# Kernel optimization log

Hardware: AMD Instinct MI355X
Metric: run time of the kernel (lower is better)

The kernel has to match this reference:

```python
import jax, jax.numpy as jnp
import numpy as np

N, F_IN, HID, HEADS, E, G, CLS = 20000, 128, 32, 8, 320000, 64, 10


def setup_inputs() -> dict:
    key = jax.random.key(0)
    ks = jax.random.split(key, 16)
    HC = HEADS * HID
    inp = {
        'x': jax.random.normal(ks[0], (N, F_IN), jnp.float32),
        'edge_index': jax.random.randint(ks[1], (2, E), 0, N, jnp.int64),
        'batch': jnp.sort(jax.random.randint(ks[2], (N,), 0, G, jnp.int64)),
        'W1': jax.random.normal(ks[3], (F_IN, HC), jnp.float32) * 0.1,
        'att_l1': jax.random.normal(ks[4], (HEADS, HID), jnp.float32) * 0.1,
        'att_r1': jax.random.normal(ks[5], (HEADS, HID), jnp.float32) * 0.1,
        'b1': jnp.zeros((HC,), jnp.float32),
        'W2': jax.random.normal(ks[6], (HC, HC), jnp.float32) * 0.1,
        'att_l2': jax.random.normal(ks[7], (HEADS, HID), jnp.float32) * 0.1,
        'att_r2': jax.random.normal(ks[8], (HEADS, HID), jnp.float32) * 0.1,
        'b2': jnp.zeros((HC,), jnp.float32),
        'lin_W': jax.random.normal(ks[9], (HC, CLS), jnp.float32) * 0.1,
        'lin_b': jnp.zeros((CLS,), jnp.float32),
    }
    return inp


def _add_self_loops(edge_index):
    loops = jnp.arange(N, dtype=edge_index.dtype)
    return (jnp.concatenate([edge_index[0], loops]),
            jnp.concatenate([edge_index[1], loops]))


def _supergat_conv(x, edge_index, W, att_l, att_r, b):
    # SuperGATConv, attention_type='MX', eval mode (no dropout / neg sampling)
    h = (x @ W).reshape(-1, HEADS, HID)          # [N, H, C]
    src, dst = _add_self_loops(edge_index)       # j -> i
    x_j = h[src]                                 # [Etot, H, C]
    x_i = h[dst]
    logits = jnp.einsum('ehc,ehc->eh', x_i, x_j)            # dot-product part
    alpha = jnp.einsum('ehc,hc->eh', x_j, att_l) + jnp.einsum('ehc,hc->eh', x_i, att_r)
    alpha = alpha * jax.nn.sigmoid(logits)
    alpha = jax.nn.leaky_relu(alpha, 0.2)
    # segment softmax over incoming edges of each dst node
    amax = jax.ops.segment_max(alpha, dst, num_segments=N)
    ex = jnp.exp(alpha - amax[dst])
    denom = jax.ops.segment_sum(ex, dst, num_segments=N)
    attn = ex / (denom[dst] + 1e-16)             # [Etot, H]
    out = jax.ops.segment_sum(x_j * attn[..., None], dst, num_segments=N)  # [N,H,C]
    return out.reshape(-1, HEADS * HID) + b


def reference(x, edge_index, batch, W1, att_l1, att_r1, b1, W2, att_l2, att_r2, b2, lin_W, lin_b):
    h = _supergat_conv(x, edge_index, W1, att_l1, att_r1, b1)
    h = jax.nn.elu(h)
    h = _supergat_conv(h, edge_index, W2, att_l2, att_r2, b2)
    # global mean pool over graphs
    sums = jax.ops.segment_sum(h, batch, num_segments=G)
    cnts = jax.ops.segment_sum(jnp.ones((h.shape[0], 1), h.dtype), batch, num_segments=G)
    pooled = sums / jnp.maximum(cnts, 1.0)
    return pooled @ lin_W + lin_b
```

## Files before the change

kernel.cpp:

```cpp
#include <hip/hip_runtime.h>
#include <hip/hip_bf16.h>
#include <math.h>

#define NNODE 20000
#define FIN   128
#define HC    256
#define HEADS 8
#define HID   32
#define NEDGE 320000
#define NGRAPH 64
#define NCLS  10
#define MAXDEG 64

typedef __attribute__((ext_vector_type(8))) short short8v;
typedef __attribute__((ext_vector_type(8))) unsigned short ushort8v;
typedef __attribute__((ext_vector_type(4))) float float4v;

__device__ __forceinline__ ushort f2bf(float f) {
    __hip_bfloat16 b = __float2bfloat16(f);
    return *(ushort*)&b;
}
__device__ __forceinline__ float bf2f(ushort u) {
    return __uint_as_float(((unsigned)u) << 16);
}


#define ZB_DEG ((NNODE + 255) / 256)
#define ZB_BND ((NNODE + 255) / 256)
#define ZB_PS  ((NGRAPH * HC + 255) / 256)

__global__ __launch_bounds__(256) void init_kernel(const float* __restrict__ W1,
                                                   const float* __restrict__ W2,
                                                   const int* __restrict__ batch,
                                                   ushort* __restrict__ W1t,
                                                   ushort* __restrict__ W2t,
                                                   int* __restrict__ deg,
                                                   int* __restrict__ gstart,
                                                   float* __restrict__ psum) {
    int b = blockIdx.x;
    if (b < 128) {
        int e = b * 256 + threadIdx.x;
        int k = e >> 8, n = e & 255;
        W1t[(long)n * FIN + k] = f2bf(W1[(long)k * 256 + n]);
    } else if (b < 384) {
        int e = (b - 128) * 256 + threadIdx.x;
        int k = e >> 8, n = e & 255;
        W2t[(long)n * HC + k] = f2bf(W2[(long)k * 256 + n]);
    } else if (b < 384 + ZB_DEG) {
        int i = (b - 384) * 256 + threadIdx.x;
        if (i < NNODE) deg[i] = 0;
    } else if (b < 384 + ZB_DEG + ZB_BND) {
        int i = (b - 384 - ZB_DEG) * 256 + threadIdx.x;
        if (i < NNODE) {
            int bi = batch[i];
            if (i == 0) {
                for (int g = 0; g <= bi; g++) gstart[g] = 0;
            } else {
                int bp = batch[i - 1];
                for (int g = bp + 1; g <= bi; g++) gstart[g] = i;
            }
            if (i == NNODE - 1) {
                for (int g = bi + 1; g <= NGRAPH; g++) gstart[g] = NNODE;
            }
        }
    } else {
        int i = (b - 384 - ZB_DEG - ZB_BND) * 256 + threadIdx.x;
        if (i < NGRAPH * HC) psum[i] = 0.f;
    }
}


__global__ __launch_bounds__(256) void fill_slots(const int* __restrict__ ei,
                                                  int* __restrict__ deg,
                                                  ushort* __restrict__ esrc) {
    int e = blockIdx.x * blockDim.x + threadIdx.x;
    if (e >= NEDGE) return;
    int src = ei[e];
    int dst = ei[NEDGE + e];
    int slot = atomicAdd(&deg[dst], 1);
    if (slot < MAXDEG) esrc[dst * MAXDEG + slot] = (ushort)src;
}


template<bool A_FP32>
__global__ __launch_bounds__(256) void gemm_mfma(const void* __restrict__ Aptr,
                                                 const ushort* __restrict__ Bt,
                                                 ushort* __restrict__ C,
                                                 const float* __restrict__ attL,
                                                 const float* __restrict__ attR,
                                                 float* __restrict__ aL,
                                                 float* __restrict__ aR,
                                                 int M, int K) {
    __shared__ __align__(16) ushort As[64][72];
    __shared__ __align__(16) ushort Bs[64][72];
    int tid = threadIdx.x;
    int rowBase = blockIdx.x * 64;
    int colBase = blockIdx.y * 64;
    int wave = tid >> 6;
    int l = tid & 63;
    int lm = l & 15;
    int quad = l >> 4;
    int r0 = (wave >> 1) * 32;
    int c0 = (wave & 1) * 32;

    float4v acc00 = {0.f, 0.f, 0.f, 0.f};
    float4v acc01 = acc00, acc10 = acc00, acc11 = acc00;

    float4  af[4];
    short8v ab[2];
    short8v bb[2];

    auto load_tile = [&](int k0) {
        if constexpr (A_FP32) {
            const float* A = (const float*)Aptr;
            #pragma unroll
            for (int q = 0; q < 4; q++) {
                int idx = tid + q * 256;
                int r   = idx >> 4;
                int kc  = (idx & 15) * 4;
                int grow = rowBase + r;
                float4 v = make_float4(0.f, 0.f, 0.f, 0.f);
                if (grow < M) v = *(const float4*)(A + (long)grow * K + k0 + kc);
                af[q] = v;
            }
        } else {
            const ushort* A = (const ushort*)Aptr;
            #pragma unroll
            for (int q = 0; q < 2; q++) {
                int ch = tid + q * 256;
                int r  = ch >> 3;
                int kc = (ch & 7) * 8;
                int grow = rowBase + r;
                short8v av = {};
                if (grow < M) av = *(const short8v*)(A + (long)grow * K + k0 + kc);
                ab[q] = av;
            }
        }
        #pragma unroll
        for (int q = 0; q < 2; q++) {
            int ch = tid + q * 256;
            int r  = ch >> 3;
            int kc = (ch & 7) * 8;
            bb[q] = *(const short8v*)(Bt + (long)(colBase + r) * K + k0 + kc);
        }
    };

    auto store_tile = [&]() {
        if constexpr (A_FP32) {
            #pragma unroll
            for (int q = 0; q < 4; q++) {
                int idx = tid + q * 256;
                int r   = idx >> 4;
                int kc  = (idx & 15) * 4;
                float4 v = af[q];
                ushort4 o = { f2bf(v.x), f2bf(v.y), f2bf(v.z), f2bf(v.w) };
                *(ushort4*)&As[r][kc] = o;
            }
        } else {
            #pragma unroll
            for (int q = 0; q < 2; q++) {
                int ch = tid + q * 256;
                int r  = ch >> 3;
                int kc = (ch & 7) * 8;
                *(short8v*)&As[r][kc] = ab[q];
            }
        }
        #pragma unroll
        for (int q = 0; q < 2; q++) {
            int ch = tid + q * 256;
            int r  = ch >> 3;
            int kc = (ch & 7) * 8;
            *(short8v*)&Bs[r][kc] = bb[q];
        }
    };

    load_tile(0);
    for (int k0 = 0; k0 < K; k0 += 64) {
        store_tile();
        __syncthreads();
        if (k0 + 64 < K) load_tile(k0 + 64);
        #pragma unroll
        for (int ks = 0; ks < 64; ks += 32) {
            int kb = ks + quad * 8;
            short8v a0 = *(const short8v*)&As[r0 + lm][kb];
            short8v a1 = *(const short8v*)&As[r0 + 16 + lm][kb];
            short8v b0 = *(const short8v*)&Bs[c0 + lm][kb];
            short8v b1 = *(const short8v*)&Bs[c0 + 16 + lm][kb];
            acc00 = __builtin_amdgcn_mfma_f32_16x16x32_bf16(a0, b0, acc00, 0, 0, 0);
            acc01 = __builtin_amdgcn_mfma_f32_16x16x32_bf16(a0, b1, acc01, 0, 0, 0);
            acc10 = __builtin_amdgcn_mfma_f32_16x16x32_bf16(a1, b0, acc10, 0, 0, 0);
            acc11 = __builtin_amdgcn_mfma_f32_16x16x32_bf16(a1, b1, acc11, 0, 0, 0);
        }
        __syncthreads();
    }

    int cb = colBase + c0;
    int hd = cb >> 5;
    float al0 = attL[cb + lm], al1 = attL[cb + 16 + lm];
    float ar0 = attR[cb + lm], ar1 = attR[cb + 16 + lm];
    #pragma unroll
    for (int mi = 0; mi < 2; mi++) {
        float4v s0 = mi ? acc10 : acc00;
        float4v s1 = mi ? acc11 : acc01;
        #pragma unroll
        for (int r = 0; r < 4; r++) {
            int row = rowBase + r0 + mi * 16 + quad * 4 + r;
            float pl = s0[r] * al0 + s1[r] * al1;
            float pr = s0[r] * ar0 + s1[r] * ar1;
            #pragma unroll
            for (int s2 = 1; s2 < 16; s2 <<= 1) {
                pl += __shfl_xor(pl, s2);
                pr += __shfl_xor(pr, s2);
            }
            if (row < M) {
                C[(long)row * 256 + cb + lm]      = f2bf(s0[r]);
                C[(long)row * 256 + cb + 16 + lm] = f2bf(s1[r]);
                if (lm == 0) {
                    aL[row * 8 + hd] = pl;
                    aR[row * 8 + hd] = pr;
                }
            }
        }
    }
}


template<int FUSE_POOL>
__global__ __launch_bounds__(256, 8) void fused_attn(const ushort* __restrict__ h,
                                                     const int* __restrict__ degv,
                                                     const ushort* __restrict__ esrc,
                                                     const float* __restrict__ aL,
                                                     const float* __restrict__ aR,
                                                     const float* __restrict__ bias,
                                                     ushort* __restrict__ out,
                                                     float* __restrict__ psum,
                                                     const int* __restrict__ batch,
                                                     int apply_elu) {
    __shared__ float sh[4][HC];
    __shared__ int sgid[4];
    int wave = threadIdx.x >> 6;
    int node = blockIdx.x * 4 + wave;
    int l = threadIdx.x & 63;
    int slot = l >> 5;
    int lh = l & 31;
    int head = lh >> 2;

    if (FUSE_POOL && l == 0) sgid[wave] = batch[node];

    const ushort8v* h8 = (const ushort8v*)h;
    ushort8v hiu = h8[(long)node * 32 + lh];
    float a_ri = aR[node * 8 + head];
    float a_li = aL[node * 8 + head];
    int beg = node * MAXDEG;
    int deg = min(degv[node], MAXDEG);

    int p  = slot;
    int j0 = (p     < deg) ? (int)esrc[beg + p]     : 0;
    int j1 = (p + 2 < deg) ? (int)esrc[beg + p + 2] : 0;
    int j2 = (p + 4 < deg) ? (int)esrc[beg + p + 4] : 0;
    ushort8v hb0 = h8[(long)j0 * 32 + lh];
    float    ab0 = aL[j0 * 8 + head];
    ushort8v hb1 = h8[(long)j1 * 32 + lh];
    float    ab1 = aL[j1 * 8 + head];

    float prod_s = 0.f;
    #pragma unroll
    for (int c = 0; c < 8; c++) {
        float v = bf2f(hiu[c]);
        prod_s = fmaf(v, v, prod_s);
    }
    prod_s += __shfl_xor(prod_s, 1);
    prod_s += __shfl_xor(prod_s, 2);
    float alpha_s = (a_li + a_ri) * __builtin_amdgcn_rcpf(1.f + __expf(-prod_s));
    alpha_s = (alpha_s > 0.f) ? alpha_s : 0.2f * alpha_s;
    float ex_s = (slot == 0) ? __expf(alpha_s) : 0.f;

    float lsum = ex_s;
    float acc[8];
    #pragma unroll
    for (int c = 0; c < 8; c++) acc[c] = ex_s * bf2f(hiu[c]);

    for (; p < deg; p += 2) {
        ushort8v hb2 = h8[(long)j2 * 32 + lh];
        float    ab2 = aL[j2 * 8 + head];
        int j3 = (p + 6 < deg) ? (int)esrc[beg + p + 6] : 0;

        float hj[8];
        float prod = 0.f;
        #pragma unroll
        for (int c = 0; c < 8; c++) {
            hj[c] = bf2f(hb0[c]);
            prod = fmaf(bf2f(hiu[c]), hj[c], prod);
        }
        prod += __shfl_xor(prod, 1);
        prod += __shfl_xor(prod, 2);
        float alpha = (ab0 + a_ri) * __builtin_amdgcn_rcpf(1.f + __expf(-prod));
        alpha = (alpha > 0.f) ? alpha : 0.2f * alpha;
        float ex = __expf(alpha);
        lsum += ex;
        #pragma unroll
        for (int c = 0; c < 8; c++) acc[c] += ex * hj[c];

        hb0 = hb1; ab0 = ab1;
        hb1 = hb2; ab1 = ab2;
        j2  = j3;
    }

    lsum += __shfl_xor(lsum, 32);
    #pragma unroll
    for (int c = 0; c < 8; c++) acc[c] += __shfl_xor(acc[c], 32);

    if (slot == 0) {
        float inv = __builtin_amdgcn_rcpf(lsum + 1e-16f);
        float4 b0 = ((const float4*)bias)[lh * 2];
        float4 b1 = ((const float4*)bias)[lh * 2 + 1];
        float bb[8] = {b0.x, b0.y, b0.z, b0.w, b1.x, b1.y, b1.z, b1.w};
        if (FUSE_POOL) {
            #pragma unroll
            for (int c = 0; c < 8; c++)
                sh[wave][lh * 8 + c] = acc[c] * inv + bb[c];
        } else {
            ushort8v o;
            #pragma unroll
            for (int c = 0; c < 8; c++) {
                float r = acc[c] * inv + bb[c];
                if (apply_elu) r = (r > 0.f) ? r : (__expf(r) - 1.f);
                o[c] = f2bf(r);
            }
            *(ushort8v*)(out + (long)node * 256 + lh * 8) = o;
        }
    }

    if (FUSE_POOL) {
        __syncthreads();
        int t = threadIdx.x;
        float v = sh[0][t];
        int g0 = sgid[0];
        #pragma unroll
        for (int w2 = 1; w2 < 4; w2++) {
            int gw = sgid[w2];
            if (gw == g0) v += sh[w2][t];
            else { atomicAdd(&psum[g0 * HC + t], v); g0 = gw; v = sh[w2][t]; }
        }
        atomicAdd(&psum[g0 * HC + t], v);
    }
}


__global__ __launch_bounds__(256) void final2(const float* __restrict__ psum,
                                              const int* __restrict__ gstart,
                                              const float* __restrict__ linW,
                                              const float* __restrict__ linb,
                                              float* __restrict__ out) {
    int g = blockIdx.x;
    int t = threadIdx.x;
    __shared__ float pooled[HC];
    float cnt = fmaxf((float)(gstart[g + 1] - gstart[g]), 1.f);
    pooled[t] = psum[g * HC + t] / cnt;
    __syncthreads();
    if (t < NCLS) {
        float o = linb[t];
        for (int c = 0; c < HC; c++) o += pooled[c] * linW[c * NCLS + t];
        out[g * NCLS + t] = o;
    }
}


extern "C" void kernel_launch(void* const* d_in, const int* in_sizes, int n_in,
                              void* d_out, int out_size, void* d_ws, size_t ws_size,
                              hipStream_t stream) {
    const float* x     = (const float*)d_in[0];
    const int*   ei    = (const int*)d_in[1];
    const int*   batch = (const int*)d_in[2];
    const float* W1    = (const float*)d_in[3];
    const float* attL1 = (const float*)d_in[4];
    const float* attR1 = (const float*)d_in[5];
    const float* b1    = (const float*)d_in[6];
    const float* W2    = (const float*)d_in[7];
    const float* attL2 = (const float*)d_in[8];
    const float* attR2 = (const float*)d_in[9];
    const float* b2    = (const float*)d_in[10];
    const float* linW  = (const float*)d_in[11];
    const float* linb  = (const float*)d_in[12];
    float* out = (float*)d_out;

    char* w = (char*)d_ws;
    size_t o = 0;
    int* deg      = (int*)(w + o); o += (size_t)NNODE * 4;
    o = (o + 15) & ~(size_t)15;
    ushort* esrc  = (ushort*)(w + o); o += (size_t)NNODE * MAXDEG * 2;
    o = (o + 15) & ~(size_t)15;
    ushort* W1t = (ushort*)(w + o); o += (size_t)FIN * HC * 2;
    ushort* W2t = (ushort*)(w + o); o += (size_t)HC * HC * 2;
    o = (o + 15) & ~(size_t)15;
    ushort* hbA = (ushort*)(w + o); o += (size_t)NNODE * HC * 2;
    ushort* hbB = (ushort*)(w + o); o += (size_t)NNODE * HC * 2;
    o = (o + 15) & ~(size_t)15;
    float* aL   = (float*)(w + o); o += (size_t)NNODE * HEADS * 4;
    float* aR   = (float*)(w + o); o += (size_t)NNODE * HEADS * 4;
    o = (o + 15) & ~(size_t)15;
    float* psum = (float*)(w + o); o += (size_t)NGRAPH * HC * 4;
    int* gstart = (int*)(w + o); o += 80 * 4;

    init_kernel<<<384 + ZB_DEG + ZB_BND + ZB_PS, 256, 0, stream>>>(
        W1, W2, batch, W1t, W2t, deg, gstart, psum);

    int eb = (NEDGE + 255) / 256;
    fill_slots<<<eb, 256, 0, stream>>>(ei, deg, esrc);

    dim3 gg((NNODE + 63) / 64, HC / 64);
    int ab = (NNODE + 3) / 4;
    gemm_mfma<true><<<gg, 256, 0, stream>>>(x, W1t, hbA, attL1, attR1, aL, aR, NNODE, FIN);
    fused_attn<0><<<ab, 256, 0, stream>>>(hbA, deg, esrc, aL, aR, b1, hbB, nullptr, batch, 1);
    gemm_mfma<false><<<gg, 256, 0, stream>>>(hbB, W2t, hbA, attL2, attR2, aL, aR, NNODE, HC);
    fused_attn<1><<<ab, 256, 0, stream>>>(hbA, deg, esrc, aL, aR, b2, nullptr, psum, batch, 0);
    final2<<<NGRAPH, 256, 0, stream>>>(psum, gstart, linW, linb, out);
}
```

Baseline: 195.1 us.

## Widen GEMM tile to full 256 columns and deepen attention gather prefetch

```diff
diff --git a/kernel.cpp b/kernel.cpp
--- a/kernel.cpp
+++ b/kernel.cpp
@@ -92,23 +92,26 @@
                                                  float* __restrict__ aR,
                                                  int M, int K) {
     __shared__ __align__(16) ushort As[64][72];
-    __shared__ __align__(16) ushort Bs[64][72];
+    __shared__ __align__(16) ushort Bs[256][72];
     int tid = threadIdx.x;
     int rowBase = blockIdx.x * 64;
-    int colBase = blockIdx.y * 64;
     int wave = tid >> 6;
     int l = tid & 63;
     int lm = l & 15;
     int quad = l >> 4;
     int r0 = (wave >> 1) * 32;
-    int c0 = (wave & 1) * 32;
-
-    float4v acc00 = {0.f, 0.f, 0.f, 0.f};
-    float4v acc01 = acc00, acc10 = acc00, acc11 = acc00;
+    int c0 = (wave & 1) * 128;
+
+    float4v acc[2][8];
+    #pragma unroll
+    for (int m = 0; m < 2; m++)
+        #pragma unroll
+        for (int n = 0; n < 8; n++)
+            acc[m][n] = (float4v){0.f, 0.f, 0.f, 0.f};
 
     float4  af[4];
     short8v ab[2];
-    short8v bb[2];
+    short8v bb[8];
 
     auto load_tile = [&](int k0) {
         if constexpr (A_FP32) {
@@ -137,11 +140,11 @@
             }
         }
         #pragma unroll
-        for (int q = 0; q < 2; q++) {
+        for (int q = 0; q < 8; q++) {
             int ch = tid + q * 256;
             int r  = ch >> 3;
             int kc = (ch & 7) * 8;
-            bb[q] = *(const short8v*)(Bt + (long)(colBase + r) * K + k0 + kc);
+            bb[q] = *(const short8v*)(Bt + (long)r * K + k0 + kc);
         }
     };
 
@@ -166,7 +169,7 @@
             }
         }
         #pragma unroll
-        for (int q = 0; q < 2; q++) {
+        for (int q = 0; q < 8; q++) {
             int ch = tid + q * 256;
             int r  = ch >> 3;
             int kc = (ch & 7) * 8;
@@ -184,40 +187,46 @@
             int kb = ks + quad * 8;
             short8v a0 = *(const short8v*)&As[r0 + lm][kb];
             short8v a1 = *(const short8v*)&As[r0 + 16 + lm][kb];
-            short8v b0 = *(const short8v*)&Bs[c0 + lm][kb];
-            short8v b1 = *(const short8v*)&Bs[c0 + 16 + lm][kb];
-            acc00 = __builtin_amdgcn_mfma_f32_16x16x32_bf16(a0, b0, acc00, 0, 0, 0);
-            acc01 = __builtin_amdgcn_mfma_f32_16x16x32_bf16(a0, b1, acc01, 0, 0, 0);
-            acc10 = __builtin_amdgcn_mfma_f32_16x16x32_bf16(a1, b0, acc10, 0, 0, 0);
-            acc11 = __builtin_amdgcn_mfma_f32_16x16x32_bf16(a1, b1, acc11, 0, 0, 0);
+            #pragma unroll
+            for (int n = 0; n < 8; n++) {
+                short8v b = *(const short8v*)&Bs[c0 + n * 16 + lm][kb];
+                acc[0][n] = __builtin_amdgcn_mfma_f32_16x16x32_bf16(a0, b, acc[0][n], 0, 0, 0);
+                acc[1][n] = __builtin_amdgcn_mfma_f32_16x16x32_bf16(a1, b, acc[1][n], 0, 0, 0);
+            }
         }
         __syncthreads();
     }
 
-    int cb = colBase + c0;
-    int hd = cb >> 5;
-    float al0 = attL[cb + lm], al1 = attL[cb + 16 + lm];
-    float ar0 = attR[cb + lm], ar1 = attR[cb + 16 + lm];
-    #pragma unroll
-    for (int mi = 0; mi < 2; mi++) {
-        float4v s0 = mi ? acc10 : acc00;
-        float4v s1 = mi ? acc11 : acc01;
+    int cb = c0;
+    int hb0 = cb >> 5;
+    float al[8], ar[8];
+    #pragma unroll
+    for (int n = 0; n < 8; n++) {
+        al[n] = attL[cb + n * 16 + lm];
+        ar[n] = attR[cb + n * 16 + lm];
+    }
+    #pragma unroll
+    for (int m = 0; m < 2; m++) {
         #pragma unroll
         for (int r = 0; r < 4; r++) {
-            int row = rowBase + r0 + mi * 16 + quad * 4 + r;
-            float pl = s0[r] * al0 + s1[r] * al1;
-            float pr = s0[r] * ar0 + s1[r] * ar1;
-            #pragma unroll
-            for (int s2 = 1; s2 < 16; s2 <<= 1) {
-                pl += __shfl_xor(pl, s2);
-                pr += __shfl_xor(pr, s2);
-            }
+            int row = rowBase + r0 + m * 16 + quad * 4 + r;
             if (row < M) {
-                C[(long)row * 256 + cb + lm]      = f2bf(s0[r]);
-                C[(long)row * 256 + cb + 16 + lm] = f2bf(s1[r]);
-                if (lm == 0) {
-                    aL[row * 8 + hd] = pl;
-                    aR[row * 8 + hd] = pr;
+                #pragma unroll
+                for (int n = 0; n < 8; n++)
+                    C[(long)row * 256 + cb + n * 16 + lm] = f2bf(acc[m][n][r]);
+                #pragma unroll
+                for (int hd = 0; hd < 4; hd++) {
+                    float pl = acc[m][2 * hd][r] * al[2 * hd] + acc[m][2 * hd + 1][r] * al[2 * hd + 1];
+                    float pr = acc[m][2 * hd][r] * ar[2 * hd] + acc[m][2 * hd + 1][r] * ar[2 * hd + 1];
+                    #pragma unroll
+                    for (int s2 = 1; s2 < 16; s2 <<= 1) {
+                        pl += __shfl_xor(pl, s2);
+                        pr += __shfl_xor(pr, s2);
+                    }
+                    if (lm == 0) {
+                        aL[row * 8 + hb0 + hd] = pl;
+                        aR[row * 8 + hb0 + hd] = pr;
+                    }
                 }
             }
         }
@@ -254,21 +263,21 @@
     int beg = node * MAXDEG;
     int deg = min(degv[node], MAXDEG);
 
+    float hi[8];
+    #pragma unroll
+    for (int c = 0; c < 8; c++) hi[c] = bf2f(hiu[c]);
+
     int p  = slot;
-    int j0 = (p     < deg) ? (int)esrc[beg + p]     : 0;
-    int j1 = (p + 2 < deg) ? (int)esrc[beg + p + 2] : 0;
-    int j2 = (p + 4 < deg) ? (int)esrc[beg + p + 4] : 0;
-    ushort8v hb0 = h8[(long)j0 * 32 + lh];
-    float    ab0 = aL[j0 * 8 + head];
-    ushort8v hb1 = h8[(long)j1 * 32 + lh];
-    float    ab1 = aL[j1 * 8 + head];
+    int jA = (p     < deg) ? (int)esrc[beg + p]     : 0;
+    int jB = (p + 2 < deg) ? (int)esrc[beg + p + 2] : 0;
+    ushort8v hA = h8[(long)jA * 32 + lh];
+    float    aA = aL[jA * 8 + head];
+    ushort8v hB = h8[(long)jB * 32 + lh];
+    float    aB = aL[jB * 8 + head];
 
     float prod_s = 0.f;
     #pragma unroll
-    for (int c = 0; c < 8; c++) {
-        float v = bf2f(hiu[c]);
-        prod_s = fmaf(v, v, prod_s);
-    }
+    for (int c = 0; c < 8; c++) prod_s = fmaf(hi[c], hi[c], prod_s);
     prod_s += __shfl_xor(prod_s, 1);
     prod_s += __shfl_xor(prod_s, 2);
     float alpha_s = (a_li + a_ri) * __builtin_amdgcn_rcpf(1.f + __expf(-prod_s));
@@ -278,33 +287,51 @@
     float lsum = ex_s;
     float acc[8];
     #pragma unroll
-    for (int c = 0; c < 8; c++) acc[c] = ex_s * bf2f(hiu[c]);
-
-    for (; p < deg; p += 2) {
-        ushort8v hb2 = h8[(long)j2 * 32 + lh];
-        float    ab2 = aL[j2 * 8 + head];
-        int j3 = (p + 6 < deg) ? (int)esrc[beg + p + 6] : 0;
-
-        float hj[8];
-        float prod = 0.f;
-        #pragma unroll
-        for (int c = 0; c < 8; c++) {
-            hj[c] = bf2f(hb0[c]);
-            prod = fmaf(bf2f(hiu[c]), hj[c], prod);
-        }
-        prod += __shfl_xor(prod, 1);
-        prod += __shfl_xor(prod, 2);
-        float alpha = (ab0 + a_ri) * __builtin_amdgcn_rcpf(1.f + __expf(-prod));
-        alpha = (alpha > 0.f) ? alpha : 0.2f * alpha;
-        float ex = __expf(alpha);
-        lsum += ex;
-        #pragma unroll
-        for (int c = 0; c < 8; c++) acc[c] += ex * hj[c];
-
-        hb0 = hb1; ab0 = ab1;
-        hb1 = hb2; ab1 = ab2;
-        j2  = j3;
-    }
+    for (int c = 0; c < 8; c++) acc[c] = ex_s * hi[c];
+
+#define CONSUME(HV, AV, VALID)                                                 \
+    {                                                                          \
+        float hj[8]; float prod = 0.f;                                         \
+        _Pragma("unroll")                                                      \
+        for (int c = 0; c < 8; c++) {                                          \
+            hj[c] = bf2f(HV[c]);                                               \
+            prod = fmaf(hi[c], hj[c], prod);                                   \
+        }                                                                      \
+        prod += __shfl_xor(prod, 1);                                           \
+        prod += __shfl_xor(prod, 2);                                           \
+        float alpha = (AV + a_ri) * __builtin_amdgcn_rcpf(1.f + __expf(-prod));\
+        alpha = (alpha > 0.f) ? alpha : 0.2f * alpha;                          \
+        float ex = (VALID) ? __expf(alpha) : 0.f;                              \
+        lsum += ex;                                                            \
+        _Pragma("unroll")                                                      \
+        for (int c = 0; c < 8; c++) acc[c] += ex * hj[c];                      \
+    }
+
+    while (p < deg) {
+        int jC = (p + 4 < deg) ? (int)esrc[beg + p + 4] : 0;
+        int jD = (p + 6 < deg) ? (int)esrc[beg + p + 6] : 0;
+        ushort8v hC = h8[(long)jC * 32 + lh];
+        float    aC = aL[jC * 8 + head];
+        ushort8v hD = h8[(long)jD * 32 + lh];
+        float    aD = aL[jD * 8 + head];
+
+        CONSUME(hA, aA, true);
+        CONSUME(hB, aB, (p + 2 < deg));
+        p += 4;
+        if (p >= deg) break;
+
+        int jA2 = (p + 4 < deg) ? (int)esrc[beg + p + 4] : 0;
+        int jB2 = (p + 6 < deg) ? (int)esrc[beg + p + 6] : 0;
+        hA = h8[(long)jA2 * 32 + lh];
+        aA = aL[jA2 * 8 + head];
+        hB = h8[(long)jB2 * 32 + lh];
+        aB = aL[jB2 * 8 + head];
+
+        CONSUME(hC, aC, true);
+        CONSUME(hD, aD, (p + 2 < deg));
+        p += 4;
+    }
+#undef CONSUME
 
     lsum += __shfl_xor(lsum, 32);
     #pragma unroll
@@ -408,7 +435,7 @@
     int eb = (NEDGE + 255) / 256;
     fill_slots<<<eb, 256, 0, stream>>>(ei, deg, esrc);
 
-    dim3 gg((NNODE + 63) / 64, HC / 64);
+    int gg = (NNODE + 63) / 64;
     int ab = (NNODE + 3) / 4;
     gemm_mfma<true><<<gg, 256, 0, stream>>>(x, W1t, hbA, attL1, attR1, aL, aR, NNODE, FIN);
     fused_attn<0><<<ab, 256, 0, stream>>>(hbA, deg, esrc, aL, aR, b1, hbB, nullptr, batch, 1);
```

Result: slower. 242.7 us (+24.4%).
